# Performance work log

Hardware: AMD Instinct MI355X
Metric: run time of the kernel (lower is better)

## Reference

```python
import jax, jax.numpy as jnp
import numpy as np

DIM = 32
ED = DIM * DIM          # 1024
HID = ED * 4            # 4096
EPS = 1e-5


def _ln(x, g, b):
    # LayerNorm over last two dims (d, d)
    m = x.mean(axis=(-2, -1), keepdims=True)
    v = jnp.var(x, axis=(-2, -1), keepdims=True)
    return (x - m) * jax.lax.rsqrt(v + EPS) * g + b


def setup_inputs() -> dict:
    key = jax.random.key(0)
    ks = jax.random.split(key, 10)
    b, s, d = 2, 1024, DIM
    inp = {
        "x": jax.random.normal(ks[0], (b, s, d, d), dtype=jnp.float32),
        # StateSpaceLayer params
        "log_A": jax.random.normal(ks[1], (d,), dtype=jnp.float32) * 0.02,
        "w_dt": jax.random.normal(ks[2], (d,), dtype=jnp.float32) / np.sqrt(d),
        "b_dt": jnp.zeros((), dtype=jnp.float32),
        "g_ssm": jnp.ones((d, d), dtype=jnp.float32),
        "b_ssm": jnp.zeros((d, d), dtype=jnp.float32),
        # FFN params
        "g_ffn": jnp.ones((d, d), dtype=jnp.float32),
        "b_ffn": jnp.zeros((d, d), dtype=jnp.float32),
        "W1": jax.random.normal(ks[3], (ED, HID), dtype=jnp.float32) / np.sqrt(ED),
        "bb1": jnp.zeros((HID,), dtype=jnp.float32),
        "W2": jax.random.normal(ks[4], (HID, ED), dtype=jnp.float32) / np.sqrt(HID),
        "bb2": jnp.zeros((ED,), dtype=jnp.float32),
    }
    return inp


def reference(x, log_A, w_dt, b_dt, g_ssm, b_ssm, g_ffn, b_ffn, W1, bb1, W2, bb2):
    b, s, d, _ = x.shape
    # ---- StateSpaceLayer (parallel / training path) ----
    xn = _ln(x, g_ssm, b_ssm)                          # (b,s,d,d)
    A_cont = -jnp.exp(log_A)                           # (d,)
    # dt_proj: Linear(d,1) over last axis, then squeeze -> (b,s,d)
    dt = jax.nn.softplus(jnp.einsum('bsrc,c->bsr', xn, w_dt) + b_dt)
    log_a = dt * A_cont                                # (b,s,d)
    cs = jnp.cumsum(log_a, axis=1)                     # (b,s,d)
    log_M = cs[:, :, None, :] - cs[:, None, :, :]      # (b,t,j,d)
    tmask = jnp.arange(s)[:, None] >= jnp.arange(s)[None, :]  # (t,j) causal
    M = jnp.where(tmask[None, :, :, None], jnp.exp(log_M), 0.0)
    ssm_out = jnp.einsum('btjr,bjrc->btrc', M, xn) + x  # residual
    # ---- MatrixFeedForward ----
    fn = _ln(ssm_out, g_ffn, b_ffn).reshape(b, s, d * d)
    h = jax.nn.gelu(fn @ W1 + bb1, approximate=False)
    y = (h @ W2 + bb2).reshape(b, s, d, d)
    return ssm_out + y
```

## Files before the change

kernel.cpp:

```cpp
#include <hip/hip_runtime.h>
#include <math.h>

#define EPSF 1e-5f

typedef __attribute__((ext_vector_type(4))) float f32x4;
typedef __attribute__((ext_vector_type(2))) long long2v;

__device__ __forceinline__ unsigned short f2bf(float f) {
  unsigned int u = __float_as_uint(f);
  u += 0x7FFFu + ((u >> 16) & 1u);
  return (unsigned short)(u >> 16);
}
__device__ __forceinline__ float bf2f(unsigned short u) {
  return __uint_as_float((unsigned int)u << 16);
}

__device__ __forceinline__ void async_load16(const void* g, void* l) {
  __builtin_amdgcn_global_load_lds(
      (const __attribute__((address_space(1))) void*)g,
      (__attribute__((address_space(3))) void*)l, 16, 0, 0);
}


__global__ __launch_bounds__(256) void k_pre(
    const float* __restrict__ x, const float* __restrict__ g, const float* __restrict__ bta,
    const float* __restrict__ w_dt, const float* __restrict__ b_dt,
    const float* __restrict__ log_A, unsigned short* __restrict__ xn, float* __restrict__ log_a,
    const float* __restrict__ W1, unsigned char* __restrict__ W1t,
    const float* __restrict__ W2, unsigned char* __restrict__ W2t) {
  __shared__ float smem[64 * 65];
  int tid = threadIdx.x;
  if (blockIdx.x < 2048) {
    int bs = blockIdx.x;
    int t = tid;
    float4 v = ((const float4*)(x + (size_t)bs * 1024))[t];
    float s = v.x + v.y + v.z + v.w;
    float ss = v.x * v.x + v.y * v.y + v.z * v.z + v.w * v.w;
    #pragma unroll
    for (int o = 1; o < 64; o <<= 1) { s += __shfl_xor(s, o); ss += __shfl_xor(ss, o); }
    float* red = smem;
    int w = t >> 6;
    if ((t & 63) == 0) { red[w] = s; red[4 + w] = ss; }
    __syncthreads();
    float S = red[0] + red[1] + red[2] + red[3];
    float SS = red[4] + red[5] + red[6] + red[7];
    float m = S * (1.0f / 1024.0f);
    float var = SS * (1.0f / 1024.0f) - m * m;
    float inv = rsqrtf(var + EPSF);
    float4 gv = ((const float4*)g)[t];
    float4 bv = ((const float4*)bta)[t];
    float4 o;
    o.x = (v.x - m) * inv * gv.x + bv.x;
    o.y = (v.y - m) * inv * gv.y + bv.y;
    o.z = (v.z - m) * inv * gv.z + bv.z;
    o.w = (v.w - m) * inv * gv.w + bv.w;
    ushort4 ob;
    ob.x = f2bf(o.x); ob.y = f2bf(o.y); ob.z = f2bf(o.z); ob.w = f2bf(o.w);
    ((ushort4*)(xn + (size_t)bs * 1024))[t] = ob;
    float4 wv = ((const float4*)w_dt)[t & 7];
    float part = o.x * wv.x + o.y * wv.y + o.z * wv.z + o.w * wv.w;
    part += __shfl_xor(part, 1);
    part += __shfl_xor(part, 2);
    part += __shfl_xor(part, 4);
    if ((t & 7) == 0) {
      int r = t >> 3;
      float z = part + b_dt[0];
      float sp = (z > 20.0f) ? z : log1pf(expf(z));
      log_a[(size_t)bs * 32 + r] = sp * (-expf(log_A[r]));
    }
  } else {
    int bid = blockIdx.x - 2048;
    bool isW1 = bid < 1024;
    const float* src; unsigned char* dst; int C, r0, c0, nkgp;
    if (isW1) { src = W1; dst = W1t; C = 4096; nkgp = 16;
                c0 = (bid & 63) * 64; r0 = (bid >> 6) * 64; }
    else { bid -= 1024; src = W2; dst = W2t; C = 1024; nkgp = 64;
           c0 = (bid & 15) * 64; r0 = (bid >> 4) * 64; }
    #pragma unroll
    for (int q = 0; q < 4; ++q) {
      int lin = q * 256 + tid;
      int r = lin >> 4, cq = lin & 15;
      float4 v = *(const float4*)(src + (size_t)(r0 + r) * C + c0 + cq * 4);
      smem[r * 65 + cq * 4 + 0] = v.x; smem[r * 65 + cq * 4 + 1] = v.y;
      smem[r * 65 + cq * 4 + 2] = v.z; smem[r * 65 + cq * 4 + 3] = v.w;
    }
    __syncthreads();
    #pragma unroll
    for (int q = 0; q < 2; ++q) {
      int lin = q * 256 + tid;
      int c = lin & 63, rh = lin >> 6;
      int n = c0 + c, k = r0 + rh * 8;
      int nt = n >> 4, l15n = n & 15;
      int kp = k >> 6, qd = (k >> 3) & 3, half = (k >> 5) & 1;
      int p0 = __builtin_amdgcn_cvt_pk_fp8_f32(
          smem[(rh * 8 + 0) * 65 + c] * 16.0f, smem[(rh * 8 + 1) * 65 + c] * 16.0f, 0, false);
      p0 = __builtin_amdgcn_cvt_pk_fp8_f32(
          smem[(rh * 8 + 2) * 65 + c] * 16.0f, smem[(rh * 8 + 3) * 65 + c] * 16.0f, p0, true);
      int p1 = __builtin_amdgcn_cvt_pk_fp8_f32(
          smem[(rh * 8 + 4) * 65 + c] * 16.0f, smem[(rh * 8 + 5) * 65 + c] * 16.0f, 0, false);
      p1 = __builtin_amdgcn_cvt_pk_fp8_f32(
          smem[(rh * 8 + 6) * 65 + c] * 16.0f, smem[(rh * 8 + 7) * 65 + c] * 16.0f, p1, true);
      int2 pk; pk.x = p0; pk.y = p1;
      *(int2*)(dst + ((size_t)(nt * nkgp + kp)) * 1024 + (qd * 16 + l15n) * 16 + half * 8) = pk;
    }
  }
}

template <int PASS>
__global__ __launch_bounds__(256) void k_scan_pass(
    const unsigned short* __restrict__ xn, const float* __restrict__ x,
    const float* __restrict__ loga, float4* __restrict__ E, float* __restrict__ P,
    const float* __restrict__ bb2, float* __restrict__ out) {
  int bx = blockIdx.x;
  int b = bx >> 8, r = (bx >> 3) & 31, ch = bx & 7;
  int tid = threadIdx.x, cg = tid & 7, sub = tid >> 3;
  __shared__ float dec[128];
  __shared__ float4 sE[32][8];
  __shared__ float sP[32];
  if (tid < 128)
    dec[tid] = expf(loga[(size_t)(b * 1024 + ch * 128 + tid) * 32 + r]);
  __syncthreads();
  int t0 = ch * 128 + sub * 4;
  size_t base = ((size_t)(b * 1024 + t0) * 1024 + r * 32 + cg * 4) >> 2;
  const ushort4* xn4 = (const ushort4*)xn;
  float4 xv[4];
  #pragma unroll
  for (int i = 0; i < 4; ++i) {
    ushort4 u = xn4[base + (size_t)i * 256];
    xv[i].x = bf2f(u.x); xv[i].y = bf2f(u.y); xv[i].z = bf2f(u.z); xv[i].w = bf2f(u.w);
  }
  float4 S = {0.f, 0.f, 0.f, 0.f};
  float Pl = 1.0f;
  #pragma unroll
  for (int i = 0; i < 4; ++i) {
    float d = dec[sub * 4 + i];
    S.x = d * S.x + xv[i].x; S.y = d * S.y + xv[i].y;
    S.z = d * S.z + xv[i].z; S.w = d * S.w + xv[i].w;
    Pl *= d;
  }
  sE[sub][cg] = S;
  if (cg == 0) sP[sub] = Pl;
  __syncthreads();
  if (PASS == 0) {
    if (tid < 8) {
      float4 Et = {0.f, 0.f, 0.f, 0.f};
      float PP = 1.0f;
      #pragma unroll
      for (int h = 0; h < 32; ++h) {
        float p = sP[h]; float4 e = sE[h][tid];
        Et.x = p * Et.x + e.x; Et.y = p * Et.y + e.y;
        Et.z = p * Et.z + e.z; Et.w = p * Et.w + e.w;
        PP *= p;
      }
      E[((size_t)(b * 32 + r) * 8 + ch) * 8 + tid] = Et;
      if (tid == 0) P[(b * 32 + r) * 8 + ch] = PP;
    }
  } else {
    float4 Sin = {0.f, 0.f, 0.f, 0.f};
    const float4* Eb = E + (size_t)(b * 32 + r) * 64 + cg;
    const float* Pb = P + (size_t)(b * 32 + r) * 8;
    for (int h = 0; h < ch; ++h) {
      float p = Pb[h]; float4 e = Eb[h * 8];
      Sin.x = p * Sin.x + e.x; Sin.y = p * Sin.y + e.y;
      Sin.z = p * Sin.z + e.z; Sin.w = p * Sin.w + e.w;
    }
    for (int h = 0; h < sub; ++h) {
      float p = sP[h]; float4 e = sE[h][cg];
      Sin.x = p * Sin.x + e.x; Sin.y = p * Sin.y + e.y;
      Sin.z = p * Sin.z + e.z; Sin.w = p * Sin.w + e.w;
    }
    float4 bb = ((const float4*)bb2)[r * 8 + cg];
    const float4* x4 = (const float4*)x;
    float4* out4 = (float4*)out;
    #pragma unroll
    for (int i = 0; i < 4; ++i) {
      float d = dec[sub * 4 + i];
      Sin.x = d * Sin.x + xv[i].x; Sin.y = d * Sin.y + xv[i].y;
      Sin.z = d * Sin.z + xv[i].z; Sin.w = d * Sin.w + xv[i].w;
      float4 rx = x4[base + (size_t)i * 256];
      float4 oi;
      oi.x = Sin.x + rx.x + bb.x; oi.y = Sin.y + rx.y + bb.y;
      oi.z = Sin.z + rx.z + bb.z; oi.w = Sin.w + rx.w + bb.w;
      out4[base + (size_t)i * 256] = oi;
    }
  }
}

__global__ __launch_bounds__(256) void k_ln2(
    const float* __restrict__ out, const float* __restrict__ bb2,
    const float* __restrict__ g, const float* __restrict__ bta,
    unsigned char* __restrict__ fn) {
  int bs = blockIdx.x;
  int t = threadIdx.x;
  float4 v = ((const float4*)(out + (size_t)bs * 1024))[t];
  float4 bb = ((const float4*)bb2)[t];
  v.x -= bb.x; v.y -= bb.y; v.z -= bb.z; v.w -= bb.w;
  float s = v.x + v.y + v.z + v.w;
  float ss = v.x * v.x + v.y * v.y + v.z * v.z + v.w * v.w;
  #pragma unroll
  for (int o = 1; o < 64; o <<= 1) { s += __shfl_xor(s, o); ss += __shfl_xor(ss, o); }
  __shared__ float red[8];
  int w = t >> 6;
  if ((t & 63) == 0) { red[w] = s; red[4 + w] = ss; }
  __syncthreads();
  float S = red[0] + red[1] + red[2] + red[3];
  float SS = red[4] + red[5] + red[6] + red[7];
  float m = S * (1.0f / 1024.0f);
  float var = SS * (1.0f / 1024.0f) - m * m;
  float inv = rsqrtf(var + EPSF);
  float4 gv = ((const float4*)g)[t];
  float4 bv = ((const float4*)bta)[t];
  float f0 = (v.x - m) * inv * gv.x + bv.x;
  float f1 = (v.y - m) * inv * gv.y + bv.y;
  float f2 = (v.z - m) * inv * gv.z + bv.z;
  float f3 = (v.w - m) * inv * gv.w + bv.w;
  int p = __builtin_amdgcn_cvt_pk_fp8_f32(f0, f1, 0, false);
  p = __builtin_amdgcn_cvt_pk_fp8_f32(f2, f3, p, true);
  int mt = bs >> 4, l15m = bs & 15;
  int kp = t >> 4, qd = (t >> 1) & 3, half = (t >> 3) & 1, j0 = (t & 1) * 4;
  *(int*)(fn + ((size_t)(mt * 16 + kp)) * 1024 + (qd * 16 + l15m) * 16 + half * 8 + j0) = p;
}

template <int EPI, int NKGP>
__global__ __launch_bounds__(256, 2) void k_gemm_lds(
    const unsigned char* __restrict__ Ap, const unsigned char* __restrict__ Bp,
    const float* __restrict__ bias, void* __restrict__ C) {
  __shared__ __align__(16) unsigned char sAB[65536];
  unsigned char* sA = sAB;
  unsigned char* sB = sAB + 32768;
  int L = blockIdx.x;
  int m0, n0, kp0;
  if (EPI == 0) {
    int xcd = L & 7;
    int nq = xcd & 3, mh = xcd >> 2;
    int rest = L >> 3;
    int nx = rest & 7, my = rest >> 3;
    n0 = (nq * 8 + nx) * 128;
    m0 = (mh * 8 + my) * 128;
    kp0 = 0;
  } else {
    int xcd = L & 7;
    int ks = xcd >> 1, mh = xcd & 1;
    int rest = L >> 3;
    int nx = rest & 7, my = rest >> 3;
    n0 = nx * 128;
    m0 = (mh * 8 + my) * 128;
    kp0 = ks * 16;
  }
  int tid = threadIdx.x;
  int wave = tid >> 6, lane = tid & 63;
  int wr = wave >> 1, wc = wave & 1;
  int l15 = lane & 15, quad = lane >> 4;
  int mt0b = m0 >> 4, nt0b = n0 >> 4;

  f32x4 zero = {0.0f, 0.0f, 0.0f, 0.0f};
  f32x4 acc[4][4];
  #pragma unroll
  for (int i = 0; i < 4; ++i)
    #pragma unroll
    for (int j = 0; j < 4; ++j) acc[i][j] = zero;

  const unsigned char* gsrc = (wave < 2) ? Ap : Bp;
  int rt0 = (wave < 2) ? mt0b : nt0b;
  unsigned char* ldst = ((wave < 2) ? sA : sB) + (wave & 1) * 16384;
  int sb0 = (wave & 1) * 16;

  #pragma unroll 1
  for (int st = 0; st < 4; ++st) {
    int kps = kp0 + st * 4;
    #pragma unroll
    for (int t = 0; t < 16; ++t) {
      int sb = sb0 + t;
      int rt = sb >> 2, kl = sb & 3;
      async_load16(gsrc + ((size_t)(rt0 + rt) * NKGP + kps + kl) * 1024 + lane * 16,
                   ldst + t * 1024);
    }
    __syncthreads();
    #pragma unroll
    for (int kl = 0; kl < 4; ++kl) {
      long2v af[4], bf[4];
      #pragma unroll
      for (int i = 0; i < 4; ++i)
        af[i] = *(const long2v*)(sA + ((wr * 4 + i) * 4 + kl) * 1024 + lane * 16);
      #pragma unroll
      for (int j = 0; j < 4; ++j)
        bf[j] = *(const long2v*)(sB + ((wc * 4 + j) * 4 + kl) * 1024 + lane * 16);
      #pragma unroll
      for (int i = 0; i < 4; ++i)
        #pragma unroll
        for (int j = 0; j < 4; ++j)
          acc[i][j] = __builtin_amdgcn_mfma_f32_16x16x32_fp8_fp8(af[i].x, bf[j].x, acc[i][j], 0, 0, 0);
      #pragma unroll
      for (int i = 0; i < 4; ++i)
        #pragma unroll
        for (int j = 0; j < 4; ++j)
          acc[i][j] = __builtin_amdgcn_mfma_f32_16x16x32_fp8_fp8(af[i].y, bf[j].y, acc[i][j], 0, 0, 0);
    }
    __syncthreads();
  }

  if (EPI == 0) {
    unsigned char* sC = sAB;
    #pragma unroll
    for (int i = 0; i < 4; ++i) {
      #pragma unroll
      for (int j = 0; j < 4; ++j) {
        int col_l = wc * 64 + j * 16 + l15;
        float bval = bias[n0 + col_l];
        int kp_l = col_l >> 6, q2 = (col_l >> 3) & 3, half2 = (col_l >> 5) & 1, j2 = col_l & 7;
        unsigned char* ld = sC + ((wr * 4 + i) * 2 + kp_l) * 1024 + q2 * 256 + half2 * 8 + j2;
        float vv[4];
        #pragma unroll
        for (int v = 0; v < 4; ++v) {
          float val = acc[i][j][v] * 0.0625f + bval;
          vv[v] = 0.5f * val * (1.0f + erff(val * 0.70710678118654752f));
        }
        int p01 = __builtin_amdgcn_cvt_pk_fp8_f32(vv[0], vv[1], 0, false);
        int p23 = __builtin_amdgcn_cvt_pk_fp8_f32(vv[2], vv[3], 0, false);
        ld[(quad * 4 + 0) * 16] = (unsigned char)(p01 & 0xff);
        ld[(quad * 4 + 1) * 16] = (unsigned char)((p01 >> 8) & 0xff);
        ld[(quad * 4 + 2) * 16] = (unsigned char)(p23 & 0xff);
        ld[(quad * 4 + 3) * 16] = (unsigned char)((p23 >> 8) & 0xff);
      }
    }
    __syncthreads();
    unsigned char* C8 = (unsigned char*)C;
    int mt2_0 = m0 >> 4, kp2_0 = n0 >> 6;
    #pragma unroll
    for (int p = 0; p < 4; ++p) {
      int ci = p * 256 + tid;
      int sb = ci >> 6, off = (ci & 63) * 16;
      int mt2 = mt2_0 + (sb >> 1), kp2 = kp2_0 + (sb & 1);
      *(int4*)(C8 + ((size_t)(mt2 * 64 + kp2)) * 1024 + off) =
          *(const int4*)(sC + sb * 1024 + off);
    }
  } else {
    float* O = (float*)C;
    #pragma unroll
    for (int i = 0; i < 4; ++i)
      #pragma unroll
      for (int j = 0; j < 4; ++j) {
        int col = n0 + wc * 64 + j * 16 + l15;
        #pragma unroll
        for (int v = 0; v < 4; ++v) {
          int row = m0 + wr * 64 + i * 16 + quad * 4 + v;
          atomicAdd(&O[(size_t)row * 1024 + col], acc[i][j][v] * 0.0625f);
        }
      }
  }
}

extern "C" void kernel_launch(void* const* d_in, const int* in_sizes, int n_in,
                              void* d_out, int out_size, void* d_ws, size_t ws_size,
                              hipStream_t stream) {
  const float* x     = (const float*)d_in[0];
  const float* log_A = (const float*)d_in[1];
  const float* w_dt  = (const float*)d_in[2];
  const float* b_dt  = (const float*)d_in[3];
  const float* g_ssm = (const float*)d_in[4];
  const float* b_ssm = (const float*)d_in[5];
  const float* g_ffn = (const float*)d_in[6];
  const float* b_ffn = (const float*)d_in[7];
  const float* W1    = (const float*)d_in[8];
  const float* bb1   = (const float*)d_in[9];
  const float* W2    = (const float*)d_in[10];
  const float* bb2   = (const float*)d_in[11];
  float* out = (float*)d_out;

  const size_t MB = 1u << 20;
  char* ws = (char*)d_ws;
  unsigned short* xn   = (unsigned short*)(ws);
  unsigned char* W1t   = (unsigned char*)(ws + 4 * MB);
  float* loga          = (float*)(ws + 8 * MB);
  float4* Ebuf         = (float4*)(ws + 8 * MB + 262144);
  float* Pbuf          = (float*)(ws + 8 * MB + 393216);
  unsigned char* fn    = (unsigned char*)(ws + 9 * MB);
  unsigned char* W2t   = (unsigned char*)(ws + 11 * MB);
  unsigned char* hbf   = (unsigned char*)(ws + 15 * MB);

  k_pre<<<4096, 256, 0, stream>>>(x, g_ssm, b_ssm, w_dt, b_dt, log_A, xn, loga,
                                  W1, W1t, W2, W2t);
  k_scan_pass<0><<<512, 256, 0, stream>>>(xn, x, loga, Ebuf, Pbuf, bb2, out);
  k_scan_pass<1><<<512, 256, 0, stream>>>(xn, x, loga, Ebuf, Pbuf, bb2, out);
  k_ln2<<<2048, 256, 0, stream>>>(out, bb2, g_ffn, b_ffn, fn);
  k_gemm_lds<0, 16><<<512, 256, 0, stream>>>(fn, W1t, bb1, (void*)hbf);
  k_gemm_lds<1, 64><<<512, 256, 0, stream>>>(hbf, W2t, nullptr, (void*)out);
}
```

Before: 175.6 us.

## Switch FP8 GEMMs to scaled 16x16x128 MFMA with matching packed layout

Replaces the 16x16x32 fp8 MFMA with the MI355 mfma_scale 16x16x128 f8f6f4 instruction, using unit scales. Weight, activation and hidden packing layouts are reorganized into 2KB blocks that each hold 128 K values, so every lane loads 32 bytes per tile. This cuts the MFMA instruction count by four per tile, targeting higher matrix throughput in both FFN GEMMs. It also changes the layout code in three kernels, and any indexing mistake there would give wrong results.

Measured after the change: 171.0 us. -2.6%, faster.

```diff
diff --git a/kernel.cpp b/kernel.cpp
--- a/kernel.cpp
+++ b/kernel.cpp
@@ -4,7 +4,8 @@
 #define EPSF 1e-5f
 
 typedef __attribute__((ext_vector_type(4))) float f32x4;
-typedef __attribute__((ext_vector_type(2))) long long2v;
+typedef __attribute__((ext_vector_type(4))) int i32x4;
+typedef __attribute__((ext_vector_type(8))) int i32x8;
 
 __device__ __forceinline__ unsigned short f2bf(float f) {
   unsigned int u = __float_as_uint(f);
@@ -71,10 +72,10 @@
   } else {
     int bid = blockIdx.x - 2048;
     bool isW1 = bid < 1024;
-    const float* src; unsigned char* dst; int C, r0, c0, nkgp;
-    if (isW1) { src = W1; dst = W1t; C = 4096; nkgp = 16;
+    const float* src; unsigned char* dst; int C, r0, c0, NK;
+    if (isW1) { src = W1; dst = W1t; C = 4096; NK = 8;
                 c0 = (bid & 63) * 64; r0 = (bid >> 6) * 64; }
-    else { bid -= 1024; src = W2; dst = W2t; C = 1024; nkgp = 64;
+    else { bid -= 1024; src = W2; dst = W2t; C = 1024; NK = 32;
            c0 = (bid & 15) * 64; r0 = (bid >> 4) * 64; }
     #pragma unroll
     for (int q = 0; q < 4; ++q) {
@@ -90,8 +91,6 @@
       int lin = q * 256 + tid;
       int c = lin & 63, rh = lin >> 6;
       int n = c0 + c, k = r0 + rh * 8;
-      int nt = n >> 4, l15n = n & 15;
-      int kp = k >> 6, qd = (k >> 3) & 3, half = (k >> 5) & 1;
       int p0 = __builtin_amdgcn_cvt_pk_fp8_f32(
           smem[(rh * 8 + 0) * 65 + c] * 16.0f, smem[(rh * 8 + 1) * 65 + c] * 16.0f, 0, false);
       p0 = __builtin_amdgcn_cvt_pk_fp8_f32(
@@ -101,7 +100,9 @@
       p1 = __builtin_amdgcn_cvt_pk_fp8_f32(
           smem[(rh * 8 + 6) * 65 + c] * 16.0f, smem[(rh * 8 + 7) * 65 + c] * 16.0f, p1, true);
       int2 pk; pk.x = p0; pk.y = p1;
-      *(int2*)(dst + ((size_t)(nt * nkgp + kp)) * 1024 + (qd * 16 + l15n) * 16 + half * 8) = pk;
+      size_t sb = (size_t)(n >> 4) * NK + (k >> 7);
+      int l = ((k >> 5) & 3) * 16 + (n & 15);
+      *(int2*)(dst + sb * 2048 + ((k >> 4) & 1) * 1024 + l * 16 + (k & 15)) = pk;
     }
   }
 }
@@ -216,12 +217,13 @@
   float f3 = (v.w - m) * inv * gv.w + bv.w;
   int p = __builtin_amdgcn_cvt_pk_fp8_f32(f0, f1, 0, false);
   p = __builtin_amdgcn_cvt_pk_fp8_f32(f2, f3, p, true);
-  int mt = bs >> 4, l15m = bs & 15;
-  int kp = t >> 4, qd = (t >> 1) & 3, half = (t >> 3) & 1, j0 = (t & 1) * 4;
-  *(int*)(fn + ((size_t)(mt * 16 + kp)) * 1024 + (qd * 16 + l15m) * 16 + half * 8 + j0) = p;
-}
-
-template <int EPI, int NKGP>
+  int k = t * 4;
+  size_t sb = (size_t)(bs >> 4) * 8 + (k >> 7);
+  int l = ((k >> 5) & 3) * 16 + (bs & 15);
+  *(int*)(fn + sb * 2048 + ((k >> 4) & 1) * 1024 + l * 16 + (k & 15)) = p;
+}
+
+template <int EPI, int NK>
 __global__ __launch_bounds__(256, 2) void k_gemm_lds(
     const unsigned char* __restrict__ Ap, const unsigned char* __restrict__ Bp,
     const float* __restrict__ bias, void* __restrict__ C) {
@@ -245,7 +247,7 @@
     int nx = rest & 7, my = rest >> 3;
     n0 = nx * 128;
     m0 = (mh * 8 + my) * 128;
-    kp0 = ks * 16;
+    kp0 = ks * 8;
   }
   int tid = threadIdx.x;
   int wave = tid >> 6, lane = tid & 63;
@@ -262,39 +264,44 @@
 
   const unsigned char* gsrc = (wave < 2) ? Ap : Bp;
   int rt0 = (wave < 2) ? mt0b : nt0b;
-  unsigned char* ldst = ((wave < 2) ? sA : sB) + (wave & 1) * 16384;
-  int sb0 = (wave & 1) * 16;
+  unsigned char* ldsb = (wave < 2) ? sA : sB;
+  int w01 = wave & 1;
 
   #pragma unroll 1
   for (int st = 0; st < 4; ++st) {
-    int kps = kp0 + st * 4;
+    int kpb = kp0 + st * 2;
     #pragma unroll
     for (int t = 0; t < 16; ++t) {
-      int sb = sb0 + t;
-      int rt = sb >> 2, kl = sb & 3;
-      async_load16(gsrc + ((size_t)(rt0 + rt) * NKGP + kps + kl) * 1024 + lane * 16,
-                   ldst + t * 1024);
-    }
-    __syncthreads();
-    #pragma unroll
-    for (int kl = 0; kl < 4; ++kl) {
-      long2v af[4], bf[4];
-      #pragma unroll
-      for (int i = 0; i < 4; ++i)
-        af[i] = *(const long2v*)(sA + ((wr * 4 + i) * 4 + kl) * 1024 + lane * 16);
-      #pragma unroll
-      for (int j = 0; j < 4; ++j)
-        bf[j] = *(const long2v*)(sB + ((wc * 4 + j) * 4 + kl) * 1024 + lane * 16);
+      int s = w01 * 8 + (t >> 1);
+      int h = t & 1;
+      int rt = s >> 1, kt = s & 1;
+      async_load16(gsrc + ((size_t)(rt0 + rt) * NK + (kpb + kt)) * 2048 + h * 1024 + lane * 16,
+                   ldsb + s * 2048 + h * 1024 + lane * 16);
+    }
+    __syncthreads();
+    #pragma unroll
+    for (int kl = 0; kl < 2; ++kl) {
+      i32x8 af[4], bf[4];
+      #pragma unroll
+      for (int i = 0; i < 4; ++i) {
+        const unsigned char* pa = sA + ((wr * 4 + i) * 2 + kl) * 2048 + lane * 16;
+        i32x4 lo = *(const i32x4*)pa;
+        i32x4 hi = *(const i32x4*)(pa + 1024);
+        af[i] = __builtin_shufflevector(lo, hi, 0, 1, 2, 3, 4, 5, 6, 7);
+      }
+      #pragma unroll
+      for (int j = 0; j < 4; ++j) {
+        const unsigned char* pb = sB + ((wc * 4 + j) * 2 + kl) * 2048 + lane * 16;
+        i32x4 lo = *(const i32x4*)pb;
+        i32x4 hi = *(const i32x4*)(pb + 1024);
+        bf[j] = __builtin_shufflevector(lo, hi, 0, 1, 2, 3, 4, 5, 6, 7);
+      }
       #pragma unroll
       for (int i = 0; i < 4; ++i)
         #pragma unroll
         for (int j = 0; j < 4; ++j)
-          acc[i][j] = __builtin_amdgcn_mfma_f32_16x16x32_fp8_fp8(af[i].x, bf[j].x, acc[i][j], 0, 0, 0);
-      #pragma unroll
-      for (int i = 0; i < 4; ++i)
-        #pragma unroll
-        for (int j = 0; j < 4; ++j)
-          acc[i][j] = __builtin_amdgcn_mfma_f32_16x16x32_fp8_fp8(af[i].y, bf[j].y, acc[i][j], 0, 0, 0);
+          acc[i][j] = __builtin_amdgcn_mfma_scale_f32_16x16x128_f8f6f4(
+              af[i], bf[j], acc[i][j], 0, 0, 0, 0x7F7F7F7F, 0, 0x7F7F7F7F);
     }
     __syncthreads();
   }
@@ -307,8 +314,9 @@
       for (int j = 0; j < 4; ++j) {
         int col_l = wc * 64 + j * 16 + l15;
         float bval = bias[n0 + col_l];
-        int kp_l = col_l >> 6, q2 = (col_l >> 3) & 3, half2 = (col_l >> 5) & 1, j2 = col_l & 7;
-        unsigned char* ld = sC + ((wr * 4 + i) * 2 + kp_l) * 1024 + q2 * 256 + half2 * 8 + j2;
+        int half2 = (col_l >> 4) & 1, lb = (col_l >> 5) & 3;
+        unsigned char* ld = sC + (wr * 4 + i) * 2048 + half2 * 1024 +
+                            (lb * 16 + quad * 4) * 16 + l15;
         float vv[4];
         #pragma unroll
         for (int v = 0; v < 4; ++v) {
@@ -317,22 +325,21 @@
         }
         int p01 = __builtin_amdgcn_cvt_pk_fp8_f32(vv[0], vv[1], 0, false);
         int p23 = __builtin_amdgcn_cvt_pk_fp8_f32(vv[2], vv[3], 0, false);
-        ld[(quad * 4 + 0) * 16] = (unsigned char)(p01 & 0xff);
-        ld[(quad * 4 + 1) * 16] = (unsigned char)((p01 >> 8) & 0xff);
-        ld[(quad * 4 + 2) * 16] = (unsigned char)(p23 & 0xff);
-        ld[(quad * 4 + 3) * 16] = (unsigned char)((p23 >> 8) & 0xff);
+        ld[0 * 16] = (unsigned char)(p01 & 0xff);
+        ld[1 * 16] = (unsigned char)((p01 >> 8) & 0xff);
+        ld[2 * 16] = (unsigned char)(p23 & 0xff);
+        ld[3 * 16] = (unsigned char)((p23 >> 8) & 0xff);
       }
     }
     __syncthreads();
     unsigned char* C8 = (unsigned char*)C;
-    int mt2_0 = m0 >> 4, kp2_0 = n0 >> 6;
+    int mt2_0 = m0 >> 4, kp2 = n0 >> 7;
     #pragma unroll
     for (int p = 0; p < 4; ++p) {
       int ci = p * 256 + tid;
-      int sb = ci >> 6, off = (ci & 63) * 16;
-      int mt2 = mt2_0 + (sb >> 1), kp2 = kp2_0 + (sb & 1);
-      *(int4*)(C8 + ((size_t)(mt2 * 64 + kp2)) * 1024 + off) =
-          *(const int4*)(sC + sb * 1024 + off);
+      int s = ci >> 7, off = (ci & 127) * 16;
+      *(int4*)(C8 + ((size_t)(mt2_0 + s) * 32 + kp2) * 2048 + off) =
+          *(const int4*)(sC + s * 2048 + off);
     }
   } else {
     float* O = (float*)C;
@@ -383,6 +390,6 @@
   k_scan_pass<0><<<512, 256, 0, stream>>>(xn, x, loga, Ebuf, Pbuf, bb2, out);
   k_scan_pass<1><<<512, 256, 0, stream>>>(xn, x, loga, Ebuf, Pbuf, bb2, out);
   k_ln2<<<2048, 256, 0, stream>>>(out, bb2, g_ffn, b_ffn, fn);
-  k_gemm_lds<0, 16><<<512, 256, 0, stream>>>(fn, W1t, bb1, (void*)hbf);
-  k_gemm_lds<1, 64><<<512, 256, 0, stream>>>(hbf, W2t, nullptr, (void*)out);
-}
+  k_gemm_lds<0, 8><<<512, 256, 0, stream>>>(fn, W1t, bb1, (void*)hbf);
+  k_gemm_lds<1, 32><<<512, 256, 0, stream>>>(hbf, W2t, nullptr, (void*)out);
+}
```
